# Kernel optimization log

Hardware: AMD Instinct MI355X
Metric: run time of the kernel (lower is better)

Reference implementation:

```python
import jax, jax.numpy as jnp
import numpy as np

B, T, H, W, C = 8, 32, 64, 64, 3
F = 24        # conv filters
U = 128       # lstm units
O = 1         # output units

def _conv(x, w, b):
    # x: [N,H,W,Cin], w: [3,3,Cin,Cout], SAME padding, linear activation
    y = jax.lax.conv_general_dilated(x, w, window_strides=(1, 1), padding='SAME',
                                     dimension_numbers=('NHWC', 'HWIO', 'NHWC'))
    return y + b

def setup_inputs() -> dict:
    key = jax.random.key(0)
    ks = jax.random.split(key, 16)
    s = lambda *shape: 0.05
    inp = {
        'x': jax.random.normal(ks[0], (B, T, H, W, C), dtype=jnp.float32),
        'conv1_w': jax.random.normal(ks[1], (3, 3, C, F), dtype=jnp.float32) * 0.1,
        'conv1_b': jnp.zeros((F,), jnp.float32),
        'conv2_w': jax.random.normal(ks[2], (3, 3, F, F), dtype=jnp.float32) * 0.1,
        'conv2_b': jnp.zeros((F,), jnp.float32),
        'Wf': jax.random.normal(ks[3], (F + U, U), dtype=jnp.float32) * 0.08,
        'bf': jnp.zeros((U,), jnp.float32),
        'Wi': jax.random.normal(ks[4], (F + U, U), dtype=jnp.float32) * 0.08,
        'bi': jnp.zeros((U,), jnp.float32),
        'Wc': jax.random.normal(ks[5], (F + U, U), dtype=jnp.float32) * 0.08,
        'bc': jnp.zeros((U,), jnp.float32),
        'Wo': jax.random.normal(ks[6], (F + U, U), dtype=jnp.float32) * 0.08,
        'bo': jnp.zeros((U,), jnp.float32),
        'out_w': jax.random.normal(ks[7], (U, O), dtype=jnp.float32) * 0.08,
        'out_b': jnp.zeros((O,), jnp.float32),
    }
    return inp

def reference(x, conv1_w, conv1_b, conv2_w, conv2_b, Wf, bf, Wi, bi, Wc, bc, Wo, bo, out_w, out_b):
    b, t, h, w, c = x.shape
    # CNN block (per-frame): two linear 3x3 convs, no pooling inside block
    xr = x.reshape(b * t, h, w, c)
    xr = _conv(xr, conv1_w, conv1_b)
    xr = _conv(xr, conv2_w, conv2_b)
    # TimeDistributed(GlobalAvgPool2D): mean over H,W -> [B,T,F]
    feat = xr.reshape(b, t, h, w, -1).mean(axis=(2, 3))

    # custom LSTM recurrence over time via scan
    def step(carry, xt):
        hs, cs = carry
        z = jnp.concatenate([xt, hs], axis=-1)           # [B, F+U]
        f = jax.nn.sigmoid(z @ Wf + bf)
        i = jax.nn.sigmoid(z @ Wi + bi)
        g = jnp.tanh(z @ Wc + bc)
        o = jax.nn.sigmoid(z @ Wo + bo)
        c_new = cs * f + i * g
        h_new = jnp.tanh(c_new) * o
        return (h_new, c_new), h_new

    h0 = jnp.zeros((b, Wf.shape[1]), x.dtype)
    c0 = jnp.zeros((b, Wf.shape[1]), x.dtype)
    _, hs = jax.lax.scan(step, (h0, c0), jnp.swapaxes(feat, 0, 1))  # [T,B,U]
    hs = jnp.swapaxes(hs, 0, 1)                                     # [B,T,U]
    return hs @ out_w + out_b                                       # [B,T,O]
```

## Files before the change

kernel.cpp:

```cpp
#include <hip/hip_runtime.h>
#include <math.h>

#define Bb 8
#define Tt 32
#define Hh 64
#define Ww 64
#define Cc 3
#define Ff 24
#define Uu 128

typedef float v2f __attribute__((ext_vector_type(2)));

__device__ __forceinline__ float fast_sigmoid(float x) {
    float e = __builtin_amdgcn_exp2f(-1.442695040888963f * x);
    return __builtin_amdgcn_rcpf(1.f + e);
}
__device__ __forceinline__ float fast_tanh(float x) {
    float e = __builtin_amdgcn_exp2f(-2.885390081777927f * x);
    return 2.f * __builtin_amdgcn_rcpf(1.f + e) - 1.f;
}

__global__ void convfeat_kernel(const float* __restrict__ x,
                                const float* __restrict__ w1, const float* __restrict__ b1,
                                const float* __restrict__ w2, const float* __restrict__ b2,
                                const float* __restrict__ Wf, const float* __restrict__ bf,
                                const float* __restrict__ Wi, const float* __restrict__ bi,
                                const float* __restrict__ Wc, const float* __restrict__ bc,
                                const float* __restrict__ Wo, const float* __restrict__ bo,
                                float* __restrict__ G) {
    int n = blockIdx.x;
    const float* xf = x + (size_t)n * (Hh * Ww * Cc);
    int tid  = threadIdx.x;
    int row  = tid >> 2;
    int part = tid & 3;

    __shared__ float partial[256][3];
    __shared__ float rowsum[64][3];
    __shared__ float colv[64][12];
    __shared__ float st[75];
    __shared__ float yst[24][9];
    __shared__ float feats[24];

    float s0 = 0.f, s1 = 0.f, s2 = 0.f;
    const float4* p4 = (const float4*)(xf + (row * Ww + part * 16) * Cc);
#pragma unroll
    for (int i = 0; i < 12; ++i) {
        float4 v = p4[i];
        int j = i * 4;
        float vv[4] = {v.x, v.y, v.z, v.w};
#pragma unroll
        for (int l = 0; l < 4; ++l) {
            int c = (j + l) % 3;
            if (c == 0) s0 += vv[l]; else if (c == 1) s1 += vv[l]; else s2 += vv[l];
        }
    }
    partial[tid][0] = s0; partial[tid][1] = s1; partial[tid][2] = s2;

    if (tid < 64) {
        int r = tid;
#pragma unroll
        for (int w4 = 0; w4 < 4; ++w4) {
            int w = (w4 < 2) ? w4 : 60 + w4;
#pragma unroll
            for (int c = 0; c < 3; ++c) colv[r][w4 * 3 + c] = xf[(r * Ww + w) * Cc + c];
        }
    }
    __syncthreads();

    if (part == 0) {
#pragma unroll
        for (int c = 0; c < 3; ++c)
            rowsum[row][c] = partial[tid][c] + partial[tid + 1][c]
                           + partial[tid + 2][c] + partial[tid + 3][c];
    }
    __syncthreads();

    if (tid < 3) {
        float t = 0.f;
        for (int r = 0; r < 64; ++r) t += rowsum[r][tid];
        st[tid * 25 + 0] = t;
    }
    if (tid >= 4 && tid < 16) {
        int k = tid - 4; int ri = k / 3, c = k % 3;
        int r = (ri < 2) ? ri : 60 + ri;
        st[c * 25 + 1 + ri] = rowsum[r][c];
    }
    if (tid >= 64 && tid < 76) {
        int k = tid - 64;
        float t = 0.f;
        for (int r = 0; r < 64; ++r) t += colv[r][k];
        int wi = k / 3, c = k % 3;
        st[c * 25 + 5 + wi] = t;
    }
    if (tid >= 128 && tid < 176) {
        int k = tid - 128; int pos = k / 3, c = k % 3;
        int ri = pos >> 2, wi = pos & 3;
        int r = (ri < 2) ? ri : 60 + ri;
        int w = (wi < 2) ? wi : 60 + wi;
        st[c * 25 + 9 + pos] = xf[(r * Ww + w) * Cc + c];
    }
    __syncthreads();

    if (tid < 24) {
        int f = tid;
        float Sy = 0, r0 = 0, r63 = 0, c0 = 0, c63 = 0, y00 = 0, y0W = 0, yH0 = 0, yHW = 0;
        for (int c = 0; c < 3; ++c) {
            const float* S = st + c * 25;
            float Sx = S[0];
            float rX[4] = {S[1], S[2], S[3], S[4]};
            float cX[4] = {S[5], S[6], S[7], S[8]};
            const float* X = S + 9;
            #define W1(p, q) w1[(((p) * 3 + (q)) * 3 + c) * 24 + f]
#pragma unroll
            for (int p = 0; p < 3; ++p)
#pragma unroll
                for (int q = 0; q < 3; ++q) {
                    float t = Sx;
                    if (p == 0) t -= rX[3];
                    if (p == 2) t -= rX[0];
                    if (q == 0) t -= cX[3];
                    if (q == 2) t -= cX[0];
                    if (p == 0 && q == 0) t += X[3 * 4 + 3];
                    if (p == 0 && q == 2) t += X[3 * 4 + 0];
                    if (p == 2 && q == 0) t += X[0 * 4 + 3];
                    if (p == 2 && q == 2) t += X[0 * 4 + 0];
                    Sy += W1(p, q) * t;
                }
#pragma unroll
            for (int q = 0; q < 3; ++q) {
                float Rr0  = rX[0] - ((q == 0) ? X[0 * 4 + 3] : 0.f) - ((q == 2) ? X[0 * 4 + 0] : 0.f);
                float Rr1  = rX[1] - ((q == 0) ? X[1 * 4 + 3] : 0.f) - ((q == 2) ? X[1 * 4 + 0] : 0.f);
                float Rr62 = rX[2] - ((q == 0) ? X[2 * 4 + 3] : 0.f) - ((q == 2) ? X[2 * 4 + 0] : 0.f);
                float Rr63 = rX[3] - ((q == 0) ? X[3 * 4 + 3] : 0.f) - ((q == 2) ? X[3 * 4 + 0] : 0.f);
                r0  += W1(1, q) * Rr0  + W1(2, q) * Rr1;
                r63 += W1(0, q) * Rr62 + W1(1, q) * Rr63;
            }
#pragma unroll
            for (int p = 0; p < 3; ++p) {
                float Rc0  = cX[0] - ((p == 0) ? X[3 * 4 + 0] : 0.f) - ((p == 2) ? X[0 * 4 + 0] : 0.f);
                float Rc1  = cX[1] - ((p == 0) ? X[3 * 4 + 1] : 0.f) - ((p == 2) ? X[0 * 4 + 1] : 0.f);
                float Rc62 = cX[2] - ((p == 0) ? X[3 * 4 + 2] : 0.f) - ((p == 2) ? X[0 * 4 + 2] : 0.f);
                float Rc63 = cX[3] - ((p == 0) ? X[3 * 4 + 3] : 0.f) - ((p == 2) ? X[0 * 4 + 3] : 0.f);
                c0  += W1(p, 1) * Rc0  + W1(p, 2) * Rc1;
                c63 += W1(p, 0) * Rc62 + W1(p, 1) * Rc63;
            }
            y00 += W1(1, 1) * X[0 * 4 + 0] + W1(1, 2) * X[0 * 4 + 1]
                 + W1(2, 1) * X[1 * 4 + 0] + W1(2, 2) * X[1 * 4 + 1];
            y0W += W1(1, 0) * X[0 * 4 + 2] + W1(1, 1) * X[0 * 4 + 3]
                 + W1(2, 0) * X[1 * 4 + 2] + W1(2, 1) * X[1 * 4 + 3];
            yH0 += W1(0, 1) * X[2 * 4 + 0] + W1(0, 2) * X[2 * 4 + 1]
                 + W1(1, 1) * X[3 * 4 + 0] + W1(1, 2) * X[3 * 4 + 1];
            yHW += W1(0, 0) * X[2 * 4 + 2] + W1(0, 1) * X[2 * 4 + 3]
                 + W1(1, 0) * X[3 * 4 + 2] + W1(1, 1) * X[3 * 4 + 3];
            #undef W1
        }
        float bb = b1[f];
        yst[f][0] = Sy + 4096.f * bb;
        yst[f][1] = r0 + 64.f * bb;
        yst[f][2] = r63 + 64.f * bb;
        yst[f][3] = c0 + 64.f * bb;
        yst[f][4] = c63 + 64.f * bb;
        yst[f][5] = y00 + bb; yst[f][6] = y0W + bb;
        yst[f][7] = yH0 + bb; yst[f][8] = yHW + bb;
    }
    __syncthreads();

    if (tid < 24) {
        int g = tid;
        float acc = 0.f;
        for (int f = 0; f < 24; ++f) {
            float Sy = yst[f][0], rY0 = yst[f][1], rY63 = yst[f][2], cY0 = yst[f][3], cY63 = yst[f][4];
            float yc00 = yst[f][5], yc0W = yst[f][6], ycH0 = yst[f][7], ycHW = yst[f][8];
#pragma unroll
            for (int p = 0; p < 3; ++p)
#pragma unroll
                for (int q = 0; q < 3; ++q) {
                    float t = Sy;
                    if (p == 0) t -= rY63;
                    if (p == 2) t -= rY0;
                    if (q == 0) t -= cY63;
                    if (q == 2) t -= cY0;
                    if (p == 0 && q == 0) t += ycHW;
                    if (p == 0 && q == 2) t += ycH0;
                    if (p == 2 && q == 0) t += yc0W;
                    if (p == 2 && q == 2) t += yc00;
                    acc += w2[(((p * 3 + q) * 24 + f) * 24) + g] * t;
                }
        }
        feats[g] = b2[g] + acc * (1.f / 4096.f);
    }
    __syncthreads();

    int b = n >> 5, t = n & 31;
    float* Gdst = G + ((size_t)(t * Bb + b)) * 512;
#pragma unroll
    for (int rep = 0; rep < 2; ++rep) {
        int col = tid + rep * 256;
        int gg = col >> 7, u = col & 127;
        const float* W    = (gg == 0) ? Wf : (gg == 1) ? Wi : (gg == 2) ? Wc : Wo;
        const float* bias = (gg == 0) ? bf : (gg == 1) ? bi : (gg == 2) ? bc : bo;
        float acc = bias[u];
#pragma unroll
        for (int k = 0; k < Ff; ++k) acc += feats[k] * W[k * Uu + u];
        Gdst[col] = acc;
    }
}

__global__ __launch_bounds__(512, 2) void lstm_kernel(
        const float* __restrict__ G,
        const float* __restrict__ Wf, const float* __restrict__ Wi,
        const float* __restrict__ Wc, const float* __restrict__ Wo,
        const float* __restrict__ out_w, const float* __restrict__ out_b,
        float* __restrict__ out) {
    int b   = blockIdx.x;
    int tid = threadIdx.x;
    int cg  = tid & 127;
    int q   = tid >> 7;
    int gate = cg >> 5;
    int c0   = (cg & 31) * 4;
    const float* Wg = (gate == 0) ? Wf : (gate == 1) ? Wi : (gate == 2) ? Wc : Wo;

    const float* wbase = Wg + (size_t)(Ff + 32 * q) * Uu + c0;
#define LDW(i) v2f a##i = *(const v2f*)(wbase + (size_t)(i) * Uu); \
               v2f b##i = *(const v2f*)(wbase + (size_t)(i) * Uu + 2)
    LDW(0);  LDW(1);  LDW(2);  LDW(3);  LDW(4);  LDW(5);  LDW(6);  LDW(7);
    LDW(8);  LDW(9);  LDW(10); LDW(11); LDW(12); LDW(13); LDW(14); LDW(15);
    LDW(16); LDW(17); LDW(18); LDW(19); LDW(20); LDW(21); LDW(22); LDW(23);
    LDW(24); LDW(25); LDW(26); LDW(27); LDW(28); LDW(29); LDW(30); LDW(31);
#undef LDW
#define KA8(p0,p1,p2,p3,p4,p5,p6,p7) asm volatile("" : "+v"(p0),"+v"(p1),\
        "+v"(p2),"+v"(p3),"+v"(p4),"+v"(p5),"+v"(p6),"+v"(p7))
    KA8(a0,b0,a1,b1,a2,b2,a3,b3);       KA8(a4,b4,a5,b5,a6,b6,a7,b7);
    KA8(a8,b8,a9,b9,a10,b10,a11,b11);   KA8(a12,b12,a13,b13,a14,b14,a15,b15);
    KA8(a16,b16,a17,b17,a18,b18,a19,b19); KA8(a20,b20,a21,b21,a22,b22,a23,b23);
    KA8(a24,b24,a25,b25,a26,b26,a27,b27); KA8(a28,b28,a29,b29,a30,b30,a31,b31);
#undef KA8

    __shared__ float Gl[Tt][512];
    __shared__ __align__(16) float hs[Uu];
    __shared__ float part[4][512];
    __shared__ float hist[Tt][Uu];

    {
        int r  = tid >> 4;
        int cc = (tid & 15) * 32;
        const float4* src = (const float4*)(G + ((size_t)(r * Bb + b)) * 512 + cc);
        float4* dst = (float4*)(&Gl[r][cc]);
#pragma unroll
        for (int i = 0; i < 8; ++i) dst[i] = src[i];
    }

    float cs = 0.f;
    if (tid < Uu) hs[tid] = 0.f;
    __syncthreads();

    for (int t = 0; t < Tt; ++t) {
        v2f ae0 = {0.f, 0.f}, ao0 = {0.f, 0.f};
        v2f ae1 = {0.f, 0.f}, ao1 = {0.f, 0.f};
        const float4* hp = (const float4*)(hs + q * 32);
#define FMA4(hq, wA0,wB0, wA1,wB1, wA2,wB2, wA3,wB3) { \
        v2f hlo = {hq.x, hq.y}; v2f hhi = {hq.z, hq.w}; \
        asm("v_pk_fma_f32 %0, %1, %2, %0 op_sel:[0,0,0] op_sel_hi:[1,0,1]" \
            : "+v"(ae0) : "v"(wA0), "v"(hlo)); \
        asm("v_pk_fma_f32 %0, %1, %2, %0 op_sel:[0,0,0] op_sel_hi:[1,0,1]" \
            : "+v"(ae1) : "v"(wB0), "v"(hlo)); \
        asm("v_pk_fma_f32 %0, %1, %2, %0 op_sel:[0,1,0] op_sel_hi:[1,1,1]" \
            : "+v"(ao0) : "v"(wA1), "v"(hlo)); \
        asm("v_pk_fma_f32 %0, %1, %2, %0 op_sel:[0,1,0] op_sel_hi:[1,1,1]" \
            : "+v"(ao1) : "v"(wB1), "v"(hlo)); \
        asm("v_pk_fma_f32 %0, %1, %2, %0 op_sel:[0,0,0] op_sel_hi:[1,0,1]" \
            : "+v"(ae0) : "v"(wA2), "v"(hhi)); \
        asm("v_pk_fma_f32 %0, %1, %2, %0 op_sel:[0,0,0] op_sel_hi:[1,0,1]" \
            : "+v"(ae1) : "v"(wB2), "v"(hhi)); \
        asm("v_pk_fma_f32 %0, %1, %2, %0 op_sel:[0,1,0] op_sel_hi:[1,1,1]" \
            : "+v"(ao0) : "v"(wA3), "v"(hhi)); \
        asm("v_pk_fma_f32 %0, %1, %2, %0 op_sel:[0,1,0] op_sel_hi:[1,1,1]" \
            : "+v"(ao1) : "v"(wB3), "v"(hhi)); }
        { float4 h0 = hp[0]; FMA4(h0, a0,b0, a1,b1, a2,b2, a3,b3); }
        { float4 h1 = hp[1]; FMA4(h1, a4,b4, a5,b5, a6,b6, a7,b7); }
        { float4 h2 = hp[2]; FMA4(h2, a8,b8, a9,b9, a10,b10, a11,b11); }
        { float4 h3 = hp[3]; FMA4(h3, a12,b12, a13,b13, a14,b14, a15,b15); }
        { float4 h4 = hp[4]; FMA4(h4, a16,b16, a17,b17, a18,b18, a19,b19); }
        { float4 h5 = hp[5]; FMA4(h5, a20,b20, a21,b21, a22,b22, a23,b23); }
        { float4 h6 = hp[6]; FMA4(h6, a24,b24, a25,b25, a26,b26, a27,b27); }
        { float4 h7 = hp[7]; FMA4(h7, a28,b28, a29,b29, a30,b30, a31,b31); }
#undef FMA4
        v2f s0 = ae0 + ao0, s1 = ae1 + ao1;
        float4 pw4; pw4.x = s0.x; pw4.y = s0.y; pw4.z = s1.x; pw4.w = s1.y;
        *(float4*)&part[q][gate * 128 + c0] = pw4;
        __syncthreads();

        if (tid < Uu) {
            int u = tid;
            float sf = part[0][u]       + part[1][u]       + part[2][u]       + part[3][u]       + Gl[t][u];
            float si = part[0][128 + u] + part[1][128 + u] + part[2][128 + u] + part[3][128 + u] + Gl[t][128 + u];
            float sg = part[0][256 + u] + part[1][256 + u] + part[2][256 + u] + part[3][256 + u] + Gl[t][256 + u];
            float so = part[0][384 + u] + part[1][384 + u] + part[2][384 + u] + part[3][384 + u] + Gl[t][384 + u];
            float f  = fast_sigmoid(sf);
            float i  = fast_sigmoid(si);
            float gg = fast_tanh(sg);
            float o  = fast_sigmoid(so);
            cs = cs * f + i * gg;
            float hn = fast_tanh(cs) * o;
            hs[u] = hn;
            hist[t][u] = hn;
        }
        __syncthreads();
    }

    int tt = tid >> 4, j = tid & 15;
    const float4* hh = (const float4*)(&hist[tt][j * 8]);
    float4 a0q = hh[0], a1q = hh[1];
    const float* owp = out_w + j * 8;
    float pw = a0q.x * owp[0] + a0q.y * owp[1] + a0q.z * owp[2] + a0q.w * owp[3]
             + a1q.x * owp[4] + a1q.y * owp[5] + a1q.z * owp[6] + a1q.w * owp[7];
#pragma unroll
    for (int off = 8; off > 0; off >>= 1) pw += __shfl_down(pw, off, 16);
    if (j == 0) out[b * Tt + tt] = pw + out_b[0];
}

extern "C" void kernel_launch(void* const* d_in, const int* in_sizes, int n_in,
                              void* d_out, int out_size, void* d_ws, size_t ws_size,
                              hipStream_t stream) {
    const float* x   = (const float*)d_in[0];
    const float* w1  = (const float*)d_in[1];
    const float* b1  = (const float*)d_in[2];
    const float* w2  = (const float*)d_in[3];
    const float* b2  = (const float*)d_in[4];
    const float* Wf  = (const float*)d_in[5];
    const float* bf  = (const float*)d_in[6];
    const float* Wi  = (const float*)d_in[7];
    const float* bi  = (const float*)d_in[8];
    const float* Wc  = (const float*)d_in[9];
    const float* bc  = (const float*)d_in[10];
    const float* Wo  = (const float*)d_in[11];
    const float* bo  = (const float*)d_in[12];
    const float* ow  = (const float*)d_in[13];
    const float* ob  = (const float*)d_in[14];
    float* out = (float*)d_out;

    float* G = (float*)d_ws;

    convfeat_kernel<<<Bb * Tt, 256, 0, stream>>>(x, w1, b1, w2, b2,
                                                 Wf, bf, Wi, bi, Wc, bc, Wo, bo, G);
    lstm_kernel<<<Bb, 512, 0, stream>>>(G, Wf, Wi, Wc, Wo, ow, ob, out);
}
```

Measured before the change: 38.57 us.

## Broadcast LSTM hidden state via readlane and halve barriers per timestep

```diff
diff --git a/kernel.cpp b/kernel.cpp
--- a/kernel.cpp
+++ b/kernel.cpp
@@ -9,8 +9,6 @@
 #define Ff 24
 #define Uu 128
 
-typedef float v2f __attribute__((ext_vector_type(2)));
-
 __device__ __forceinline__ float fast_sigmoid(float x) {
     float e = __builtin_amdgcn_exp2f(-1.442695040888963f * x);
     return __builtin_amdgcn_rcpf(1.f + e);
@@ -18,6 +16,10 @@
 __device__ __forceinline__ float fast_tanh(float x) {
     float e = __builtin_amdgcn_exp2f(-2.885390081777927f * x);
     return 2.f * __builtin_amdgcn_rcpf(1.f + e) - 1.f;
+}
+__device__ __forceinline__ float rl(float v, int lane) {
+    return __builtin_bit_cast(float,
+        __builtin_amdgcn_readlane(__builtin_bit_cast(int, v), lane));
 }
 
 __global__ void convfeat_kernel(const float* __restrict__ x,
@@ -202,11 +204,13 @@
         float acc = bias[u];
 #pragma unroll
         for (int k = 0; k < Ff; ++k) acc += feats[k] * W[k * Uu + u];
-        Gdst[col] = acc;
-    }
-}
-
-__global__ __launch_bounds__(512, 2) void lstm_kernel(
+        Gdst[u * 4 + gg] = acc;
+    }
+}
+
+__global__ __launch_bounds__(512)
+__attribute__((amdgpu_waves_per_eu(2, 2)))
+void lstm_kernel(
         const float* __restrict__ G,
         const float* __restrict__ Wf, const float* __restrict__ Wi,
         const float* __restrict__ Wc, const float* __restrict__ Wo,
@@ -214,32 +218,34 @@
         float* __restrict__ out) {
     int b   = blockIdx.x;
     int tid = threadIdx.x;
-    int cg  = tid & 127;
-    int q   = tid >> 7;
-    int gate = cg >> 5;
-    int c0   = (cg & 31) * 4;
-    const float* Wg = (gate == 0) ? Wf : (gate == 1) ? Wi : (gate == 2) ? Wc : Wo;
-
-    const float* wbase = Wg + (size_t)(Ff + 32 * q) * Uu + c0;
-#define LDW(i) v2f a##i = *(const v2f*)(wbase + (size_t)(i) * Uu); \
-               v2f b##i = *(const v2f*)(wbase + (size_t)(i) * Uu + 2)
-    LDW(0);  LDW(1);  LDW(2);  LDW(3);  LDW(4);  LDW(5);  LDW(6);  LDW(7);
-    LDW(8);  LDW(9);  LDW(10); LDW(11); LDW(12); LDW(13); LDW(14); LDW(15);
-    LDW(16); LDW(17); LDW(18); LDW(19); LDW(20); LDW(21); LDW(22); LDW(23);
-    LDW(24); LDW(25); LDW(26); LDW(27); LDW(28); LDW(29); LDW(30); LDW(31);
-#undef LDW
-#define KA8(p0,p1,p2,p3,p4,p5,p6,p7) asm volatile("" : "+v"(p0),"+v"(p1),\
-        "+v"(p2),"+v"(p3),"+v"(p4),"+v"(p5),"+v"(p6),"+v"(p7))
-    KA8(a0,b0,a1,b1,a2,b2,a3,b3);       KA8(a4,b4,a5,b5,a6,b6,a7,b7);
-    KA8(a8,b8,a9,b9,a10,b10,a11,b11);   KA8(a12,b12,a13,b13,a14,b14,a15,b15);
-    KA8(a16,b16,a17,b17,a18,b18,a19,b19); KA8(a20,b20,a21,b21,a22,b22,a23,b23);
-    KA8(a24,b24,a25,b25,a26,b26,a27,b27); KA8(a28,b28,a29,b29,a30,b30,a31,b31);
-#undef KA8
-
-    __shared__ float Gl[Tt][512];
-    __shared__ __align__(16) float hs[Uu];
-    __shared__ float part[4][512];
-    __shared__ float hist[Tt][Uu];
+    int w   = tid >> 6;
+    int l   = tid & 63;
+    int q   = w >> 1;
+    int uc  = ((w & 1) << 6) | l;
+
+    const float* Wfp = Wf + (size_t)(Ff + 32 * q) * Uu + uc;
+    const float* Wip = Wi + (size_t)(Ff + 32 * q) * Uu + uc;
+    const float* Wcp = Wc + (size_t)(Ff + 32 * q) * Uu + uc;
+    const float* Wop = Wo + (size_t)(Ff + 32 * q) * Uu + uc;
+#define LDWX(r) float wf##r = Wfp[(size_t)(r) * Uu]; \
+                float wi##r = Wip[(size_t)(r) * Uu]; \
+                float wc##r = Wcp[(size_t)(r) * Uu]; \
+                float wo##r = Wop[(size_t)(r) * Uu]
+    LDWX(0);  LDWX(1);  LDWX(2);  LDWX(3);  LDWX(4);  LDWX(5);  LDWX(6);  LDWX(7);
+    LDWX(8);  LDWX(9);  LDWX(10); LDWX(11); LDWX(12); LDWX(13); LDWX(14); LDWX(15);
+    LDWX(16); LDWX(17); LDWX(18); LDWX(19); LDWX(20); LDWX(21); LDWX(22); LDWX(23);
+    LDWX(24); LDWX(25); LDWX(26); LDWX(27); LDWX(28); LDWX(29); LDWX(30); LDWX(31);
+#undef LDWX
+#define KAW(r) asm volatile("" : "+v"(wf##r), "+v"(wi##r), "+v"(wc##r), "+v"(wo##r))
+    KAW(0);  KAW(1);  KAW(2);  KAW(3);  KAW(4);  KAW(5);  KAW(6);  KAW(7);
+    KAW(8);  KAW(9);  KAW(10); KAW(11); KAW(12); KAW(13); KAW(14); KAW(15);
+    KAW(16); KAW(17); KAW(18); KAW(19); KAW(20); KAW(21); KAW(22); KAW(23);
+    KAW(24); KAW(25); KAW(26); KAW(27); KAW(28); KAW(29); KAW(30); KAW(31);
+#undef KAW
+
+    __shared__ __align__(16) float Gl[Tt][Uu * 4];
+    __shared__ __align__(16) float part[2][4][Uu][4];
+    __shared__ __align__(16) float hist[Tt][Uu];
 
     {
         int r  = tid >> 4;
@@ -249,64 +255,50 @@
 #pragma unroll
         for (int i = 0; i < 8; ++i) dst[i] = src[i];
     }
-
+    float hn = 0.f;
     float cs = 0.f;
-    if (tid < Uu) hs[tid] = 0.f;
-    __syncthreads();
-
+    __syncthreads();
+
+#pragma clang loop unroll(disable)
     for (int t = 0; t < Tt; ++t) {
-        v2f ae0 = {0.f, 0.f}, ao0 = {0.f, 0.f};
-        v2f ae1 = {0.f, 0.f}, ao1 = {0.f, 0.f};
-        const float4* hp = (const float4*)(hs + q * 32);
-#define FMA4(hq, wA0,wB0, wA1,wB1, wA2,wB2, wA3,wB3) { \
-        v2f hlo = {hq.x, hq.y}; v2f hhi = {hq.z, hq.w}; \
-        asm("v_pk_fma_f32 %0, %1, %2, %0 op_sel:[0,0,0] op_sel_hi:[1,0,1]" \
-            : "+v"(ae0) : "v"(wA0), "v"(hlo)); \
-        asm("v_pk_fma_f32 %0, %1, %2, %0 op_sel:[0,0,0] op_sel_hi:[1,0,1]" \
-            : "+v"(ae1) : "v"(wB0), "v"(hlo)); \
-        asm("v_pk_fma_f32 %0, %1, %2, %0 op_sel:[0,1,0] op_sel_hi:[1,1,1]" \
-            : "+v"(ao0) : "v"(wA1), "v"(hlo)); \
-        asm("v_pk_fma_f32 %0, %1, %2, %0 op_sel:[0,1,0] op_sel_hi:[1,1,1]" \
-            : "+v"(ao1) : "v"(wB1), "v"(hlo)); \
-        asm("v_pk_fma_f32 %0, %1, %2, %0 op_sel:[0,0,0] op_sel_hi:[1,0,1]" \
-            : "+v"(ae0) : "v"(wA2), "v"(hhi)); \
-        asm("v_pk_fma_f32 %0, %1, %2, %0 op_sel:[0,0,0] op_sel_hi:[1,0,1]" \
-            : "+v"(ae1) : "v"(wB2), "v"(hhi)); \
-        asm("v_pk_fma_f32 %0, %1, %2, %0 op_sel:[0,1,0] op_sel_hi:[1,1,1]" \
-            : "+v"(ao0) : "v"(wA3), "v"(hhi)); \
-        asm("v_pk_fma_f32 %0, %1, %2, %0 op_sel:[0,1,0] op_sel_hi:[1,1,1]" \
-            : "+v"(ao1) : "v"(wB3), "v"(hhi)); }
-        { float4 h0 = hp[0]; FMA4(h0, a0,b0, a1,b1, a2,b2, a3,b3); }
-        { float4 h1 = hp[1]; FMA4(h1, a4,b4, a5,b5, a6,b6, a7,b7); }
-        { float4 h2 = hp[2]; FMA4(h2, a8,b8, a9,b9, a10,b10, a11,b11); }
-        { float4 h3 = hp[3]; FMA4(h3, a12,b12, a13,b13, a14,b14, a15,b15); }
-        { float4 h4 = hp[4]; FMA4(h4, a16,b16, a17,b17, a18,b18, a19,b19); }
-        { float4 h5 = hp[5]; FMA4(h5, a20,b20, a21,b21, a22,b22, a23,b23); }
-        { float4 h6 = hp[6]; FMA4(h6, a24,b24, a25,b25, a26,b26, a27,b27); }
-        { float4 h7 = hp[7]; FMA4(h7, a28,b28, a29,b29, a30,b30, a31,b31); }
-#undef FMA4
-        v2f s0 = ae0 + ao0, s1 = ae1 + ao1;
-        float4 pw4; pw4.x = s0.x; pw4.y = s0.y; pw4.z = s1.x; pw4.w = s1.y;
-        *(float4*)&part[q][gate * 128 + c0] = pw4;
+        float sf = 0.f, si = 0.f, sg = 0.f, so = 0.f;
+#define STEPR(r) { float hr = rl(hn, r); \
+        sf = fmaf(wf##r, hr, sf); si = fmaf(wi##r, hr, si); \
+        sg = fmaf(wc##r, hr, sg); so = fmaf(wo##r, hr, so); }
+        STEPR(0);  STEPR(1);  STEPR(2);  STEPR(3);
+        STEPR(4);  STEPR(5);  STEPR(6);  STEPR(7);
+        STEPR(8);  STEPR(9);  STEPR(10); STEPR(11);
+        STEPR(12); STEPR(13); STEPR(14); STEPR(15);
+        STEPR(16); STEPR(17); STEPR(18); STEPR(19);
+        STEPR(20); STEPR(21); STEPR(22); STEPR(23);
+        STEPR(24); STEPR(25); STEPR(26); STEPR(27);
+        STEPR(28); STEPR(29); STEPR(30); STEPR(31);
+#undef STEPR
+        float4 pv; pv.x = sf; pv.y = si; pv.z = sg; pv.w = so;
+        *(float4*)&part[t & 1][q][uc][0] = pv;
         __syncthreads();
 
-        if (tid < Uu) {
-            int u = tid;
-            float sf = part[0][u]       + part[1][u]       + part[2][u]       + part[3][u]       + Gl[t][u];
-            float si = part[0][128 + u] + part[1][128 + u] + part[2][128 + u] + part[3][128 + u] + Gl[t][128 + u];
-            float sg = part[0][256 + u] + part[1][256 + u] + part[2][256 + u] + part[3][256 + u] + Gl[t][256 + u];
-            float so = part[0][384 + u] + part[1][384 + u] + part[2][384 + u] + part[3][384 + u] + Gl[t][384 + u];
-            float f  = fast_sigmoid(sf);
-            float i  = fast_sigmoid(si);
-            float gg = fast_tanh(sg);
-            float o  = fast_sigmoid(so);
-            cs = cs * f + i * gg;
-            float hn = fast_tanh(cs) * o;
-            hs[u] = hn;
-            hist[t][u] = hn;
-        }
-        __syncthreads();
-    }
+        if (l < 32) {
+            int u = (q << 5) | l;
+            const float4 p0 = *(const float4*)&part[t & 1][0][u][0];
+            const float4 p1 = *(const float4*)&part[t & 1][1][u][0];
+            const float4 p2 = *(const float4*)&part[t & 1][2][u][0];
+            const float4 p3 = *(const float4*)&part[t & 1][3][u][0];
+            const float4 gv = *(const float4*)&Gl[t][u * 4];
+            float zf = p0.x + p1.x + p2.x + p3.x + gv.x;
+            float zi = p0.y + p1.y + p2.y + p3.y + gv.y;
+            float zg = p0.z + p1.z + p2.z + p3.z + gv.z;
+            float zo = p0.w + p1.w + p2.w + p3.w + gv.w;
+            float ff = fast_sigmoid(zf);
+            float ii = fast_sigmoid(zi);
+            float gg = fast_tanh(zg);
+            float oo = fast_sigmoid(zo);
+            cs = cs * ff + ii * gg;
+            hn = fast_tanh(cs) * oo;
+            if (!(w & 1)) hist[t][u] = hn;
+        }
+    }
+    __syncthreads();
 
     int tt = tid >> 4, j = tid & 15;
     const float4* hh = (const float4*)(&hist[tt][j * 8]);
```

Measured after the change: 40.71 us. +5.6%, slower.
